# Kernel tuning notes

Measured on AMD Instinct MI355X. Metric: run time of the kernel, lower is better.

The kernel has to match this reference:

```python
import jax, jax.numpy as jnp
import numpy as np

N_HEAD = 12

def setup_inputs() -> dict:
    key = jax.random.key(0)
    k1, k2, k3 = jax.random.split(key, 3)
    B, T, C = 8, 1024, 768
    x = jax.random.normal(k1, (B, T, C), dtype=jnp.float32)
    # Linear weights stored as [in, out] so y = x @ W + b (same math as torch Linear)
    w_attn = jax.random.normal(k2, (C, 3 * C), dtype=jnp.float32) * (1.0 / np.sqrt(C))
    b_attn = jnp.zeros((3 * C,), dtype=jnp.float32)
    w_proj = jax.random.normal(k3, (C, C), dtype=jnp.float32) * (1.0 / np.sqrt(C))
    b_proj = jnp.zeros((C,), dtype=jnp.float32)
    return {"x": x, "w_attn": w_attn, "b_attn": b_attn, "w_proj": w_proj, "b_proj": b_proj}

def reference(x, w_attn, b_attn, w_proj, b_proj):
    B, T, C = x.shape
    H = N_HEAD
    D = C // H
    qkv = x @ w_attn + b_attn                        # [B,T,3C]
    q, k, v = jnp.split(qkv, 3, axis=-1)             # each [B,T,C]
    q = q.reshape(B, T, H, D).transpose(0, 2, 1, 3)  # [B,H,T,D]
    k = k.reshape(B, T, H, D).transpose(0, 2, 1, 3)
    v = v.reshape(B, T, H, D).transpose(0, 2, 1, 3)
    scale = 1.0 / jnp.sqrt(jnp.asarray(D, dtype=x.dtype))
    att = jnp.einsum('bhqd,bhkd->bhqk', q, k) * scale  # [B,H,T,T]
    causal = jnp.tril(jnp.ones((T, T), dtype=bool))    # [T,T]
    att = jnp.where(causal[None, None], att, jnp.asarray(-jnp.inf, dtype=att.dtype))
    att = jax.nn.softmax(att, axis=-1)
    out = jnp.einsum('bhqk,bhkd->bhqd', att, v)        # [B,H,T,D]
    out = out.transpose(0, 2, 1, 3).reshape(B, T, C)
    return out @ w_proj + b_proj
```

## Files before the change

### kernel.cpp

```cpp
#include <hip/hip_runtime.h>
#include <hip/hip_bf16.h>
#include <cmath>

#define B_ 8
#define T_ 1024
#define C_ 768
#define H_ 12
#define D_ 64
#define N3C 2304
#define M_ 8192

typedef __bf16 bf16x4 __attribute__((ext_vector_type(4)));
typedef __bf16 bf16x8 __attribute__((ext_vector_type(8)));
typedef float  f32x4  __attribute__((ext_vector_type(4)));

typedef const __attribute__((address_space(1))) void* gptr_t;
typedef __attribute__((address_space(3))) void* lptr_t;

#define LOG2E 1.44269504088896f

__device__ __forceinline__ bf16x8 cvt_bf16x8(const float4& a, const float4& b) {
    bf16x8 r;
    r[0] = (__bf16)a.x; r[1] = (__bf16)a.y; r[2] = (__bf16)a.z; r[3] = (__bf16)a.w;
    r[4] = (__bf16)b.x; r[5] = (__bf16)b.y; r[6] = (__bf16)b.z; r[7] = (__bf16)b.w;
    return r;
}

__global__ __launch_bounds__(256) void prepass(const float* __restrict__ x,
                                               __bf16* __restrict__ xb,
                                               const float* __restrict__ wa,
                                               __bf16* __restrict__ wat,
                                               const float* __restrict__ wp,
                                               __bf16* __restrict__ wpt) {
    __shared__ float tile[32][33];
    const int bx = blockIdx.x, tid = threadIdx.x;
    if (bx < 3072) {
        int i = (bx * 256 + tid) * 8;
        float4 a = *(const float4*)&x[i];
        float4 b = *(const float4*)&x[i + 4];
        *(bf16x8*)&xb[i] = cvt_bf16x8(a, b);
        return;
    }
    const float* w;
    __bf16* wt;
    int K, N, n0, k0;
    if (bx < 4800) {
        int bb = bx - 3072;
        w = wa; wt = wat; K = 768; N = 2304;
        n0 = (bb % 72) * 32; k0 = (bb / 72) * 32;
    } else {
        int bb = bx - 4800;
        w = wp; wt = wpt; K = 768; N = 768;
        n0 = (bb % 24) * 32; k0 = (bb / 24) * 32;
    }
    int tx = tid & 31, ty = tid >> 5;
#pragma unroll
    for (int i = 0; i < 4; i++)
        tile[ty + i * 8][tx] = w[(size_t)(k0 + ty + i * 8) * N + n0 + tx];
    __syncthreads();
#pragma unroll
    for (int i = 0; i < 4; i++)
        wt[(size_t)(n0 + ty + i * 8) * K + k0 + tx] = (__bf16)tile[tx][ty + i * 8];
}

__global__ __launch_bounds__(256) void qkv_gemm_mfma(const __bf16* __restrict__ A,
                                                     const __bf16* __restrict__ Bt,
                                                     const float* __restrict__ bias,
                                                     __bf16* __restrict__ qb,
                                                     __bf16* __restrict__ kb,
                                                     __bf16* __restrict__ vbt) {
    __shared__ __bf16 smem[128 * 136];
    __bf16* As = smem;
    __bf16* Bs = smem + 8192;
    const int tid = threadIdx.x;
    const int wave = tid >> 6, lane = tid & 63;
    const int lane15 = lane & 15, quad = lane >> 4;
    const int bid = blockIdx.x;
    const int m0 = ((bid & 7) * 8 + ((bid >> 3) & 7)) * 128;
    const int n0 = (bid >> 6) * 128;
    const int wm = (wave >> 1) * 64, wn = (wave & 1) * 64;
    f32x4 acc[4][4] = {};

#define QSTAGE(KC)                                                                  \
    {                                                                               \
        const int k0s = (KC) * 64;                                                  \
        _Pragma("unroll")                                                           \
        for (int r = 0; r < 4; ++r) {                                               \
            int p = r * 256 + tid;                                                  \
            int mrow = p >> 3, csw = p & 7;                                         \
            int ksrc = (csw ^ (mrow & 7)) * 8;                                      \
            __builtin_amdgcn_global_load_lds(                                       \
                (gptr_t)(A + (size_t)(m0 + mrow) * 768 + k0s + ksrc),               \
                (lptr_t)(As + (r * 256 + wave * 64) * 8), 16, 0, 0);                \
            __builtin_amdgcn_global_load_lds(                                       \
                (gptr_t)(Bt + (size_t)(n0 + mrow) * 768 + k0s + ksrc),              \
                (lptr_t)(Bs + (r * 256 + wave * 64) * 8), 16, 0, 0);                \
        }                                                                           \
    }

    for (int kc = 0; kc < 12; ++kc) {
        QSTAGE(kc);
        __syncthreads();
#pragma unroll
        for (int ks = 0; ks < 2; ++ks) {
            bf16x8 af[4], bf[4];
#pragma unroll
            for (int mt = 0; mt < 4; ++mt) {
                int m = wm + mt * 16 + lane15;
                int csw = (ks * 4 + quad) ^ (m & 7);
                af[mt] = *(const bf16x8*)(As + m * 64 + csw * 8);
            }
#pragma unroll
            for (int nt = 0; nt < 4; ++nt) {
                int n = wn + nt * 16 + lane15;
                int csw = (ks * 4 + quad) ^ (n & 7);
                bf[nt] = *(const bf16x8*)(Bs + n * 64 + csw * 8);
            }
#pragma unroll
            for (int mt = 0; mt < 4; ++mt)
#pragma unroll
                for (int nt = 0; nt < 4; ++nt)
                    acc[mt][nt] = __builtin_amdgcn_mfma_f32_16x16x32_bf16(af[mt], bf[nt], acc[mt][nt], 0, 0, 0);
        }
        __syncthreads();
    }

    if (n0 < 1536) {
        const bool isq = (n0 < 768);
        const float sc = isq ? (0.125f * LOG2E) : 1.0f;
#pragma unroll
        for (int nt = 0; nt < 4; ++nt) {
            int n = n0 + wn + nt * 16 + lane15;
            int rem = isq ? n : (n - 768);
            int h = rem >> 6;
            int d = n & 63;
            float bv = bias[n];
            __bf16* dst = isq ? qb : kb;
#pragma unroll
            for (int mt = 0; mt < 4; ++mt) {
#pragma unroll
                for (int reg = 0; reg < 4; ++reg) {
                    int mr = m0 + wm + mt * 16 + quad * 4 + reg;
                    int bb = mr >> 10, t = mr & 1023;
                    dst[(((size_t)bb * H_ + h) * T_ + t) * D_ + d] =
                        (__bf16)((acc[mt][nt][reg] + bv) * sc);
                }
            }
        }
    } else {
        __bf16* vls = smem;
#pragma unroll
        for (int nt = 0; nt < 4; ++nt) {
            int nl = wn + nt * 16 + lane15;
            float bv = bias[n0 + nl];
#pragma unroll
            for (int mt = 0; mt < 4; ++mt)
#pragma unroll
                for (int reg = 0; reg < 4; ++reg)
                    vls[nl * 136 + wm + mt * 16 + quad * 4 + reg] =
                        (__bf16)(acc[mt][nt][reg] + bv);
        }
        __syncthreads();
        int nl = tid >> 1;
        int t0 = (tid & 1) * 64;
        int n = n0 + nl;
        int h = (n - 1536) >> 6;
        int d = n & 63;
        int bb = m0 >> 10, tg = (m0 & 1023) + t0;
        __bf16* dst = vbt + (((size_t)bb * H_ + h) * D_ + d) * T_ + tg;
        const __bf16* srcl = vls + nl * 136 + t0;
#pragma unroll
        for (int c = 0; c < 8; ++c) {
            bf16x8 v;
#pragma unroll
            for (int i = 0; i < 8; ++i) {
                int s = c * 8 + i;
                v[i] = srcl[(s & 3) * 16 + (s >> 2)];
            }
            *(bf16x8*)(dst + c * 8) = v;
        }
    }
}

__global__ __launch_bounds__(256) void proj_gemm_mfma(const __bf16* __restrict__ A,
                                                      const __bf16* __restrict__ Bt,
                                                      const float* __restrict__ bias,
                                                      float* __restrict__ out) {
    __shared__ __bf16 As[128 * 64];
    __shared__ __bf16 Bs[64 * 64];
    const int tid = threadIdx.x;
    const int wave = tid >> 6, lane = tid & 63;
    const int lane15 = lane & 15, quad = lane >> 4;
    const int bid = blockIdx.x;
    const int m0 = ((bid & 7) * 8 + ((bid >> 3) & 7)) * 128;
    const int n0 = (bid >> 6) * 64;
    const int wm = wave * 32;
    f32x4 acc[2][4] = {};

#define PSTAGE(KC)                                                                  \
    {                                                                               \
        const int k0s = (KC) * 64;                                                  \
        _Pragma("unroll")                                                           \
        for (int r = 0; r < 4; ++r) {                                               \
            int p = r * 256 + tid;                                                  \
            int mrow = p >> 3, csw = p & 7;                                         \
            int ksrc = (csw ^ (mrow & 7)) * 8;                                      \
            __builtin_amdgcn_global_load_lds(                                       \
                (gptr_t)(A + (size_t)(m0 + mrow) * 768 + k0s + ksrc),               \
                (lptr_t)(&As[0] + (r * 256 + wave * 64) * 8), 16, 0, 0);            \
        }                                                                           \
        _Pragma("unroll")                                                           \
        for (int r = 0; r < 2; ++r) {                                               \
            int p = r * 256 + tid;                                                  \
            int nrow = p >> 3, csw = p & 7;                                         \
            int ksrc = (csw ^ (nrow & 7)) * 8;                                      \
            __builtin_amdgcn_global_load_lds(                                       \
                (gptr_t)(Bt + (size_t)(n0 + nrow) * 768 + k0s + ksrc),              \
                (lptr_t)(&Bs[0] + (r * 256 + wave * 64) * 8), 16, 0, 0);            \
        }                                                                           \
    }

    for (int kc = 0; kc < 12; ++kc) {
        PSTAGE(kc);
        __syncthreads();
#pragma unroll
        for (int ks = 0; ks < 2; ++ks) {
            bf16x8 af[2], bf[4];
#pragma unroll
            for (int mt = 0; mt < 2; ++mt) {
                int m = wm + mt * 16 + lane15;
                int csw = (ks * 4 + quad) ^ (m & 7);
                af[mt] = *(const bf16x8*)(&As[0] + m * 64 + csw * 8);
            }
#pragma unroll
            for (int nt = 0; nt < 4; ++nt) {
                int n = nt * 16 + lane15;
                int csw = (ks * 4 + quad) ^ (n & 7);
                bf[nt] = *(const bf16x8*)(&Bs[0] + n * 64 + csw * 8);
            }
#pragma unroll
            for (int mt = 0; mt < 2; ++mt)
#pragma unroll
                for (int nt = 0; nt < 4; ++nt)
                    acc[mt][nt] = __builtin_amdgcn_mfma_f32_16x16x32_bf16(af[mt], bf[nt], acc[mt][nt], 0, 0, 0);
        }
        __syncthreads();
    }

#pragma unroll
    for (int nt = 0; nt < 4; ++nt) {
        int n = n0 + nt * 16 + lane15;
        float bv = bias[n];
#pragma unroll
        for (int mt = 0; mt < 2; ++mt) {
#pragma unroll
            for (int reg = 0; reg < 4; ++reg) {
                int mr = m0 + wm + mt * 16 + quad * 4 + reg;
                out[(size_t)mr * C_ + n] = acc[mt][nt][reg] + bv;
            }
        }
    }
}

__global__ __launch_bounds__(256) void attn_mfma(const __bf16* __restrict__ qb,
                                                 const __bf16* __restrict__ kb,
                                                 const __bf16* __restrict__ vbt,
                                                 __bf16* __restrict__ ao) {
    __shared__ __bf16 Ks[2][64 * 64];
    __shared__ __bf16 Vts[2][64 * 64];
    __shared__ __bf16 Ps[4 * 32 * 72];

    const int tid = threadIdx.x;
    const int wave = tid >> 6, lane = tid & 63;
    const int lane15 = lane & 15, quad = lane >> 4;
    const int bh = blockIdx.x;
    const int qt = 7 - blockIdx.y;
    const int b = bh / H_, h = bh % H_;
    const int q0 = qt * 128;

    const __bf16* Kb = kb + (size_t)bh * T_ * D_;
    const __bf16* Vb = vbt + (size_t)bh * D_ * T_;
    __bf16* Pw = Ps + wave * 32 * 72;

    bf16x8 qf[2][2];
#pragma unroll
    for (int g = 0; g < 2; ++g) {
        const __bf16* qrow = qb + ((size_t)bh * T_ + q0 + wave * 32 + g * 16 + lane15) * D_ + quad * 8;
        qf[g][0] = *(const bf16x8*)qrow;
        qf[g][1] = *(const bf16x8*)(qrow + 32);
    }

    f32x4 o[2][4] = {};
    float lsum[2][4] = {};

    const int kunits = 2 * qt + 2;

#define ASTAGE(KU, BUF)                                                            \
    {                                                                              \
        const int k0s = (KU) * 64;                                                 \
        _Pragma("unroll")                                                          \
        for (int r = 0; r < 2; ++r) {                                              \
            int p = r * 256 + tid;                                                 \
            int row = p >> 3, c = p & 7;                                           \
            int cs = (c ^ (row & 7)) * 8;                                          \
            __builtin_amdgcn_global_load_lds(                                      \
                (gptr_t)(Kb + (size_t)(k0s + row) * D_ + cs),                      \
                (lptr_t)(&Ks[BUF][0] + (r * 256 + wave * 64) * 8), 16, 0, 0);      \
            __builtin_amdgcn_global_load_lds(                                      \
                (gptr_t)(Vb + (size_t)row * T_ + k0s + cs),                        \
                (lptr_t)(&Vts[BUF][0] + (r * 256 + wave * 64) * 8), 16, 0, 0);     \
        }                                                                          \
    }

    ASTAGE(0, 0);

    for (int ku = 0; ku < kunits; ++ku) {
        __syncthreads();
        if (ku + 1 < kunits) ASTAGE(ku + 1, (ku + 1) & 1);
        const __bf16* Kc = &Ks[ku & 1][0];
        const __bf16* Vc = &Vts[ku & 1][0];
        const int k0 = ku * 64;

        f32x4 s[2][4];
#pragma unroll
        for (int kt = 0; kt < 4; ++kt) {
            int row = kt * 16 + lane15;
            bf16x8 kf0 = *(const bf16x8*)(Kc + row * 64 + ((quad) ^ (row & 7)) * 8);
            bf16x8 kf1 = *(const bf16x8*)(Kc + row * 64 + ((4 + quad) ^ (row & 7)) * 8);
#pragma unroll
            for (int g = 0; g < 2; ++g) {
                f32x4 t = {};
                t = __builtin_amdgcn_mfma_f32_16x16x32_bf16(qf[g][0], kf0, t, 0, 0, 0);
                t = __builtin_amdgcn_mfma_f32_16x16x32_bf16(qf[g][1], kf1, t, 0, 0, 0);
                s[g][kt] = t;
            }
        }

        const bool diag = (ku >= 2 * qt);
#pragma unroll
        for (int g = 0; g < 2; ++g) {
#pragma unroll
            for (int r = 0; r < 4; ++r) {
                bf16x4 pk;
#pragma unroll
                for (int kt = 0; kt < 4; ++kt) {
                    int col = k0 + kt * 16 + lane15;
                    float p = __builtin_amdgcn_exp2f(s[g][kt][r]);
                    if (diag) {
                        int qrow = q0 + wave * 32 + g * 16 + quad * 4 + r;
                        if (col > qrow) p = 0.f;
                    }
                    lsum[g][r] += p;
                    pk[kt] = (__bf16)p;
                }
                *(bf16x4*)(Pw + (g * 16 + quad * 4 + r) * 72 + lane15 * 4) = pk;
            }
        }

        bf16x8 vf[4][2];
#pragma unroll
        for (int dt = 0; dt < 4; ++dt) {
            int row = dt * 16 + lane15;
#pragma unroll
            for (int half = 0; half < 2; ++half)
                vf[dt][half] = *(const bf16x8*)(Vc + row * 64 + ((half * 4 + quad) ^ (row & 7)) * 8);
        }
#pragma unroll
        for (int g = 0; g < 2; ++g) {
#pragma unroll
            for (int half = 0; half < 2; ++half) {
                bf16x8 pf = *(const bf16x8*)(Pw + (g * 16 + lane15) * 72 + half * 32 + quad * 8);
#pragma unroll
                for (int dt = 0; dt < 4; ++dt)
                    o[g][dt] = __builtin_amdgcn_mfma_f32_16x16x32_bf16(pf, vf[dt][half], o[g][dt], 0, 0, 0);
            }
        }
    }

#pragma unroll
    for (int g = 0; g < 2; ++g) {
        float inv[4];
#pragma unroll
        for (int r = 0; r < 4; ++r) {
            float ls = lsum[g][r];
            ls += __shfl_xor(ls, 1);
            ls += __shfl_xor(ls, 2);
            ls += __shfl_xor(ls, 4);
            ls += __shfl_xor(ls, 8);
            inv[r] = 1.0f / ls;
        }
#pragma unroll
        for (int dt = 0; dt < 4; ++dt) {
#pragma unroll
            for (int r = 0; r < 4; ++r) {
                int t = q0 + wave * 32 + g * 16 + quad * 4 + r;
                ao[((size_t)(b * T_ + t)) * C_ + h * 64 + dt * 16 + lane15] =
                    (__bf16)(o[g][dt][r] * inv[r]);
            }
        }
    }
}

extern "C" void kernel_launch(void* const* d_in, const int* in_sizes, int n_in,
                              void* d_out, int out_size, void* d_ws, size_t ws_size,
                              hipStream_t stream) {
    const float* x = (const float*)d_in[0];
    const float* w_attn = (const float*)d_in[1];
    const float* b_attn = (const float*)d_in[2];
    const float* w_proj = (const float*)d_in[3];
    const float* b_proj = (const float*)d_in[4];
    float* out = (float*)d_out;

    __bf16* xb = (__bf16*)d_ws;
    __bf16* wat = xb + (size_t)M_ * C_;
    __bf16* wpt = wat + (size_t)N3C * C_;
    __bf16* qb = wpt + (size_t)C_ * C_;
    __bf16* kb = qb + (size_t)96 * T_ * D_;
    __bf16* vbt = kb + (size_t)96 * T_ * D_;
    __bf16* ao = vbt + (size_t)96 * T_ * D_;

    prepass<<<5376, 256, 0, stream>>>(x, xb, w_attn, wat, w_proj, wpt);
    qkv_gemm_mfma<<<1152, 256, 0, stream>>>(xb, wat, b_attn, qb, kb, vbt);
    attn_mfma<<<dim3(96, 8), 256, 0, stream>>>(qb, kb, vbt, ao);
    proj_gemm_mfma<<<768, 256, 0, stream>>>(ao, wpt, b_proj, out);
}
```

Before: 182.7 us.

## Restructure QKV GEMM into 256x128 tiles with triple-buffered async LDS pipeline

The QKV projection GEMM now uses 512-thread blocks computing 256x128 tiles, with a three-stage LDS ring buffer filled by direct global-to-LDS loads two k-chunks ahead. The k-loop is split into four phases that interleave LDS fragment reads, prefetch issue, raw s_barrier and MFMA bursts under raised wave priority, with explicit vmcnt waits replacing full __syncthreads. The block index mapping is re-swizzled for the new grid. The goal is to hide global load latency behind MFMA work and increase operand reuse, at the cost of much larger shared memory (144KB) and occupancy limited to at most two blocks per CU.

```diff
diff --git a/kernel.cpp b/kernel.cpp
--- a/kernel.cpp
+++ b/kernel.cpp
@@ -63,66 +63,132 @@
         wt[(size_t)(n0 + ty + i * 8) * K + k0 + tx] = (__bf16)tile[tx][ty + i * 8];
 }
 
-__global__ __launch_bounds__(256) void qkv_gemm_mfma(const __bf16* __restrict__ A,
-                                                     const __bf16* __restrict__ Bt,
-                                                     const float* __restrict__ bias,
-                                                     __bf16* __restrict__ qb,
-                                                     __bf16* __restrict__ kb,
-                                                     __bf16* __restrict__ vbt) {
-    __shared__ __bf16 smem[128 * 136];
-    __bf16* As = smem;
-    __bf16* Bs = smem + 8192;
+__global__ __launch_bounds__(512, 2) void qkv_gemm_mfma(const __bf16* __restrict__ A,
+                                                        const __bf16* __restrict__ Bt,
+                                                        const float* __restrict__ bias,
+                                                        __bf16* __restrict__ qb,
+                                                        __bf16* __restrict__ kb,
+                                                        __bf16* __restrict__ vbt) {
+    __shared__ __bf16 smem[73728];
+    __bf16* Abuf = smem;
+    __bf16* Bbuf = smem + 49152;
     const int tid = threadIdx.x;
     const int wave = tid >> 6, lane = tid & 63;
     const int lane15 = lane & 15, quad = lane >> 4;
-    const int bid = blockIdx.x;
-    const int m0 = ((bid & 7) * 8 + ((bid >> 3) & 7)) * 128;
-    const int n0 = (bid >> 6) * 128;
+    const int swz = (blockIdx.x & 7) * 72 + (blockIdx.x >> 3);
+    const int n0 = (swz % 18) * 128;
+    const int m0 = (swz / 18) * 256;
     const int wm = (wave >> 1) * 64, wn = (wave & 1) * 64;
     f32x4 acc[4][4] = {};
 
-#define QSTAGE(KC)                                                                  \
+#define ISSUE_A2(KC, R0)                                                            \
     {                                                                               \
         const int k0s = (KC) * 64;                                                  \
+        __bf16* Ad = Abuf + ((KC) % 3) * 16384;                                     \
         _Pragma("unroll")                                                           \
-        for (int r = 0; r < 4; ++r) {                                               \
-            int p = r * 256 + tid;                                                  \
-            int mrow = p >> 3, csw = p & 7;                                         \
-            int ksrc = (csw ^ (mrow & 7)) * 8;                                      \
+        for (int r = (R0); r < (R0) + 2; ++r) {                                     \
+            int p = r * 512 + tid;                                                  \
+            int row = p >> 3, csw = p & 7;                                          \
             __builtin_amdgcn_global_load_lds(                                       \
-                (gptr_t)(A + (size_t)(m0 + mrow) * 768 + k0s + ksrc),               \
-                (lptr_t)(As + (r * 256 + wave * 64) * 8), 16, 0, 0);                \
-            __builtin_amdgcn_global_load_lds(                                       \
-                (gptr_t)(Bt + (size_t)(n0 + mrow) * 768 + k0s + ksrc),              \
-                (lptr_t)(Bs + (r * 256 + wave * 64) * 8), 16, 0, 0);                \
+                (gptr_t)(A + (size_t)(m0 + row) * 768 + k0s + (csw ^ (row & 7)) * 8), \
+                (lptr_t)(Ad + (r * 512 + wave * 64) * 8), 16, 0, 0);                \
         }                                                                           \
     }
 
+#define ISSUE_B1(KC, R0)                                                            \
+    {                                                                               \
+        const int k0s = (KC) * 64;                                                  \
+        __bf16* Bd = Bbuf + ((KC) % 3) * 8192;                                      \
+        int p = (R0) * 512 + tid;                                                   \
+        int row = p >> 3, csw = p & 7;                                              \
+        __builtin_amdgcn_global_load_lds(                                           \
+            (gptr_t)(Bt + (size_t)(n0 + row) * 768 + k0s + (csw ^ (row & 7)) * 8),  \
+            (lptr_t)(Bd + ((R0) * 512 + wave * 64) * 8), 16, 0, 0);                 \
+    }
+
+#define BAR() asm volatile("s_barrier" ::: "memory")
+
+    ISSUE_A2(0, 0); ISSUE_A2(0, 2); ISSUE_B1(0, 0); ISSUE_B1(0, 1);
+    ISSUE_A2(1, 0); ISSUE_A2(1, 2); ISSUE_B1(1, 0); ISSUE_B1(1, 1);
+
     for (int kc = 0; kc < 12; ++kc) {
-        QSTAGE(kc);
-        __syncthreads();
-#pragma unroll
-        for (int ks = 0; ks < 2; ++ks) {
-            bf16x8 af[4], bf[4];
-#pragma unroll
-            for (int mt = 0; mt < 4; ++mt) {
-                int m = wm + mt * 16 + lane15;
-                int csw = (ks * 4 + quad) ^ (m & 7);
-                af[mt] = *(const bf16x8*)(As + m * 64 + csw * 8);
-            }
-#pragma unroll
-            for (int nt = 0; nt < 4; ++nt) {
-                int n = wn + nt * 16 + lane15;
-                int csw = (ks * 4 + quad) ^ (n & 7);
-                bf[nt] = *(const bf16x8*)(Bs + n * 64 + csw * 8);
-            }
-#pragma unroll
-            for (int mt = 0; mt < 4; ++mt)
-#pragma unroll
-                for (int nt = 0; nt < 4; ++nt)
-                    acc[mt][nt] = __builtin_amdgcn_mfma_f32_16x16x32_bf16(af[mt], bf[nt], acc[mt][nt], 0, 0, 0);
-        }
-        __syncthreads();
+        if (kc < 11) { asm volatile("s_waitcnt vmcnt(6)" ::: "memory"); }
+        else         { asm volatile("s_waitcnt vmcnt(0)" ::: "memory"); }
+        BAR();
+        const __bf16* Ac = Abuf + (kc % 3) * 16384;
+        const __bf16* Bc = Bbuf + (kc % 3) * 8192;
+        const bool pf = (kc + 2 < 12);
+
+        bf16x8 af[4], bfr[2];
+#pragma unroll
+        for (int mt = 0; mt < 4; ++mt) {
+            int m = wm + mt * 16 + lane15;
+            af[mt] = *(const bf16x8*)(Ac + m * 64 + (quad ^ (m & 7)) * 8);
+        }
+#pragma unroll
+        for (int nt = 0; nt < 2; ++nt) {
+            int n = wn + nt * 16 + lane15;
+            bfr[nt] = *(const bf16x8*)(Bc + n * 64 + (quad ^ (n & 7)) * 8);
+        }
+        if (pf) ISSUE_A2(kc + 2, 0);
+        BAR();
+        __builtin_amdgcn_s_setprio(1);
+#pragma unroll
+        for (int mt = 0; mt < 4; ++mt)
+#pragma unroll
+            for (int nt = 0; nt < 2; ++nt)
+                acc[mt][nt] = __builtin_amdgcn_mfma_f32_16x16x32_bf16(af[mt], bfr[nt], acc[mt][nt], 0, 0, 0);
+        __builtin_amdgcn_s_setprio(0);
+
+#pragma unroll
+        for (int nt = 0; nt < 2; ++nt) {
+            int n = wn + (2 + nt) * 16 + lane15;
+            bfr[nt] = *(const bf16x8*)(Bc + n * 64 + (quad ^ (n & 7)) * 8);
+        }
+        if (pf) ISSUE_A2(kc + 2, 2);
+        BAR();
+        __builtin_amdgcn_s_setprio(1);
+#pragma unroll
+        for (int mt = 0; mt < 4; ++mt)
+#pragma unroll
+            for (int nt = 0; nt < 2; ++nt)
+                acc[mt][2 + nt] = __builtin_amdgcn_mfma_f32_16x16x32_bf16(af[mt], bfr[nt], acc[mt][2 + nt], 0, 0, 0);
+        __builtin_amdgcn_s_setprio(0);
+
+#pragma unroll
+        for (int mt = 0; mt < 4; ++mt) {
+            int m = wm + mt * 16 + lane15;
+            af[mt] = *(const bf16x8*)(Ac + m * 64 + ((4 + quad) ^ (m & 7)) * 8);
+        }
+#pragma unroll
+        for (int nt = 0; nt < 2; ++nt) {
+            int n = wn + nt * 16 + lane15;
+            bfr[nt] = *(const bf16x8*)(Bc + n * 64 + ((4 + quad) ^ (n & 7)) * 8);
+        }
+        if (pf) ISSUE_B1(kc + 2, 0);
+        BAR();
+        __builtin_amdgcn_s_setprio(1);
+#pragma unroll
+        for (int mt = 0; mt < 4; ++mt)
+#pragma unroll
+            for (int nt = 0; nt < 2; ++nt)
+                acc[mt][nt] = __builtin_amdgcn_mfma_f32_16x16x32_bf16(af[mt], bfr[nt], acc[mt][nt], 0, 0, 0);
+        __builtin_amdgcn_s_setprio(0);
+
+#pragma unroll
+        for (int nt = 0; nt < 2; ++nt) {
+            int n = wn + (2 + nt) * 16 + lane15;
+            bfr[nt] = *(const bf16x8*)(Bc + n * 64 + ((4 + quad) ^ (n & 7)) * 8);
+        }
+        if (pf) ISSUE_B1(kc + 2, 1);
+        BAR();
+        __builtin_amdgcn_s_setprio(1);
+#pragma unroll
+        for (int mt = 0; mt < 4; ++mt)
+#pragma unroll
+            for (int nt = 0; nt < 2; ++nt)
+                acc[mt][2 + nt] = __builtin_amdgcn_mfma_f32_16x16x32_bf16(af[mt], bfr[nt], acc[mt][2 + nt], 0, 0, 0);
+        __builtin_amdgcn_s_setprio(0);
     }
 
     if (n0 < 1536) {
@@ -157,18 +223,18 @@
             for (int mt = 0; mt < 4; ++mt)
 #pragma unroll
                 for (int reg = 0; reg < 4; ++reg)
-                    vls[nl * 136 + wm + mt * 16 + quad * 4 + reg] =
+                    vls[nl * 264 + wm + mt * 16 + quad * 4 + reg] =
                         (__bf16)(acc[mt][nt][reg] + bv);
         }
         __syncthreads();
-        int nl = tid >> 1;
-        int t0 = (tid & 1) * 64;
+        int nl = tid >> 2;
+        int t0 = (tid & 3) * 64;
         int n = n0 + nl;
         int h = (n - 1536) >> 6;
         int d = n & 63;
         int bb = m0 >> 10, tg = (m0 & 1023) + t0;
         __bf16* dst = vbt + (((size_t)bb * H_ + h) * D_ + d) * T_ + tg;
-        const __bf16* srcl = vls + nl * 136 + t0;
+        const __bf16* srcl = vls + nl * 264 + t0;
 #pragma unroll
         for (int c = 0; c < 8; ++c) {
             bf16x8 v;
@@ -180,6 +246,9 @@
             *(bf16x8*)(dst + c * 8) = v;
         }
     }
+#undef ISSUE_A2
+#undef ISSUE_B1
+#undef BAR
 }
 
 __global__ __launch_bounds__(256) void proj_gemm_mfma(const __bf16* __restrict__ A,
@@ -420,7 +489,7 @@
     __bf16* ao = vbt + (size_t)96 * T_ * D_;
 
     prepass<<<5376, 256, 0, stream>>>(x, xb, w_attn, wat, w_proj, wpt);
-    qkv_gemm_mfma<<<1152, 256, 0, stream>>>(xb, wat, b_attn, qb, kb, vbt);
+    qkv_gemm_mfma<<<576, 512, 0, stream>>>(xb, wat, b_attn, qb, kb, vbt);
     attn_mfma<<<dim3(96, 8), 256, 0, stream>>>(qb, kb, vbt, ao);
     proj_gemm_mfma<<<768, 256, 0, stream>>>(ao, wpt, b_proj, out);
 }
```

Result: faster. 170.4 us (-6.7%).

## Triple-buffer QKV GEMM with async LDS loads and 256x128 tiles

Applied to the files above, without the earlier changes.

The QKV GEMM now uses 512-thread blocks computing 256x128 tiles, with a three-stage LDS ring filled by global_load_lds, so chunks kc+1 and kc+2 stream in while chunk kc is being computed. It waits on vmcnt with manual counts instead of double __syncthreads, raises wave priority around the MFMA section, and re-swizzles the block-to-tile mapping. This is meant to hide global load latency and improve reuse of A and B tiles. In exchange it uses about 144KB of LDS per block, which limits occupancy, and relies on hand-written waitcnt values being correct.

```diff
diff --git a/kernel.cpp b/kernel.cpp
--- a/kernel.cpp
+++ b/kernel.cpp
@@ -63,66 +63,80 @@
         wt[(size_t)(n0 + ty + i * 8) * K + k0 + tx] = (__bf16)tile[tx][ty + i * 8];
 }
 
-__global__ __launch_bounds__(256) void qkv_gemm_mfma(const __bf16* __restrict__ A,
-                                                     const __bf16* __restrict__ Bt,
-                                                     const float* __restrict__ bias,
-                                                     __bf16* __restrict__ qb,
-                                                     __bf16* __restrict__ kb,
-                                                     __bf16* __restrict__ vbt) {
-    __shared__ __bf16 smem[128 * 136];
-    __bf16* As = smem;
-    __bf16* Bs = smem + 8192;
+__global__ __launch_bounds__(512, 2) void qkv_gemm_mfma(const __bf16* __restrict__ A,
+                                                        const __bf16* __restrict__ Bt,
+                                                        const float* __restrict__ bias,
+                                                        __bf16* __restrict__ qb,
+                                                        __bf16* __restrict__ kb,
+                                                        __bf16* __restrict__ vbt) {
+    __shared__ __bf16 smem[73728];
+    __bf16* Abuf = smem;
+    __bf16* Bbuf = smem + 49152;
     const int tid = threadIdx.x;
     const int wave = tid >> 6, lane = tid & 63;
     const int lane15 = lane & 15, quad = lane >> 4;
-    const int bid = blockIdx.x;
-    const int m0 = ((bid & 7) * 8 + ((bid >> 3) & 7)) * 128;
-    const int n0 = (bid >> 6) * 128;
+    const int swz = (blockIdx.x & 7) * 72 + (blockIdx.x >> 3);
+    const int n0 = (swz % 18) * 128;
+    const int m0 = (swz / 18) * 256;
     const int wm = (wave >> 1) * 64, wn = (wave & 1) * 64;
     f32x4 acc[4][4] = {};
 
-#define QSTAGE(KC)                                                                  \
+#define ISSUE6(KC)                                                                  \
     {                                                                               \
         const int k0s = (KC) * 64;                                                  \
+        __bf16* Ad = Abuf + ((KC) % 3) * 16384;                                     \
+        __bf16* Bd = Bbuf + ((KC) % 3) * 8192;                                      \
         _Pragma("unroll")                                                           \
         for (int r = 0; r < 4; ++r) {                                               \
-            int p = r * 256 + tid;                                                  \
-            int mrow = p >> 3, csw = p & 7;                                         \
-            int ksrc = (csw ^ (mrow & 7)) * 8;                                      \
+            int p = r * 512 + tid;                                                  \
+            int row = p >> 3, csw = p & 7;                                          \
             __builtin_amdgcn_global_load_lds(                                       \
-                (gptr_t)(A + (size_t)(m0 + mrow) * 768 + k0s + ksrc),               \
-                (lptr_t)(As + (r * 256 + wave * 64) * 8), 16, 0, 0);                \
+                (gptr_t)(A + (size_t)(m0 + row) * 768 + k0s + (csw ^ (row & 7)) * 8), \
+                (lptr_t)(Ad + (r * 512 + wave * 64) * 8), 16, 0, 0);                \
+        }                                                                           \
+        _Pragma("unroll")                                                           \
+        for (int r = 0; r < 2; ++r) {                                               \
+            int p = r * 512 + tid;                                                  \
+            int row = p >> 3, csw = p & 7;                                          \
             __builtin_amdgcn_global_load_lds(                                       \
-                (gptr_t)(Bt + (size_t)(n0 + mrow) * 768 + k0s + ksrc),              \
-                (lptr_t)(Bs + (r * 256 + wave * 64) * 8), 16, 0, 0);                \
+                (gptr_t)(Bt + (size_t)(n0 + row) * 768 + k0s + (csw ^ (row & 7)) * 8), \
+                (lptr_t)(Bd + (r * 512 + wave * 64) * 8), 16, 0, 0);                \
         }                                                                           \
     }
 
+    ISSUE6(0);
+    ISSUE6(1);
+
     for (int kc = 0; kc < 12; ++kc) {
-        QSTAGE(kc);
-        __syncthreads();
+        if (kc < 11) { asm volatile("s_waitcnt vmcnt(6)" ::: "memory"); }
+        else         { asm volatile("s_waitcnt vmcnt(0)" ::: "memory"); }
+        asm volatile("s_barrier" ::: "memory");
+        if (kc + 2 < 12) ISSUE6(kc + 2);
+        const __bf16* Ac = Abuf + (kc % 3) * 16384;
+        const __bf16* Bc = Bbuf + (kc % 3) * 8192;
+        __builtin_amdgcn_s_setprio(1);
 #pragma unroll
         for (int ks = 0; ks < 2; ++ks) {
-            bf16x8 af[4], bf[4];
+            bf16x8 af[4], bfr[4];
 #pragma unroll
             for (int mt = 0; mt < 4; ++mt) {
                 int m = wm + mt * 16 + lane15;
                 int csw = (ks * 4 + quad) ^ (m & 7);
-                af[mt] = *(const bf16x8*)(As + m * 64 + csw * 8);
+                af[mt] = *(const bf16x8*)(Ac + m * 64 + csw * 8);
             }
 #pragma unroll
             for (int nt = 0; nt < 4; ++nt) {
                 int n = wn + nt * 16 + lane15;
                 int csw = (ks * 4 + quad) ^ (n & 7);
-                bf[nt] = *(const bf16x8*)(Bs + n * 64 + csw * 8);
+                bfr[nt] = *(const bf16x8*)(Bc + n * 64 + csw * 8);
             }
 #pragma unroll
             for (int mt = 0; mt < 4; ++mt)
 #pragma unroll
                 for (int nt = 0; nt < 4; ++nt)
-                    acc[mt][nt] = __builtin_amdgcn_mfma_f32_16x16x32_bf16(af[mt], bf[nt], acc[mt][nt], 0, 0, 0);
-        }
-        __syncthreads();
+                    acc[mt][nt] = __builtin_amdgcn_mfma_f32_16x16x32_bf16(af[mt], bfr[nt], acc[mt][nt], 0, 0, 0);
+        }
+        __builtin_amdgcn_s_setprio(0);
     }
 
     if (n0 < 1536) {
@@ -148,6 +162,7 @@
             }
         }
     } else {
+        __syncthreads();
         __bf16* vls = smem;
 #pragma unroll
         for (int nt = 0; nt < 4; ++nt) {
@@ -157,18 +172,18 @@
             for (int mt = 0; mt < 4; ++mt)
 #pragma unroll
                 for (int reg = 0; reg < 4; ++reg)
-                    vls[nl * 136 + wm + mt * 16 + quad * 4 + reg] =
+                    vls[nl * 264 + wm + mt * 16 + quad * 4 + reg] =
                         (__bf16)(acc[mt][nt][reg] + bv);
         }
         __syncthreads();
-        int nl = tid >> 1;
-        int t0 = (tid & 1) * 64;
+        int nl = tid >> 2;
+        int t0 = (tid & 3) * 64;
         int n = n0 + nl;
         int h = (n - 1536) >> 6;
         int d = n & 63;
         int bb = m0 >> 10, tg = (m0 & 1023) + t0;
         __bf16* dst = vbt + (((size_t)bb * H_ + h) * D_ + d) * T_ + tg;
-        const __bf16* srcl = vls + nl * 136 + t0;
+        const __bf16* srcl = vls + nl * 264 + t0;
 #pragma unroll
         for (int c = 0; c < 8; ++c) {
             bf16x8 v;
@@ -180,6 +195,7 @@
             *(bf16x8*)(dst + c * 8) = v;
         }
     }
+#undef ISSUE6
 }
 
 __global__ __launch_bounds__(256) void proj_gemm_mfma(const __bf16* __restrict__ A,
@@ -420,7 +436,7 @@
     __bf16* ao = vbt + (size_t)96 * T_ * D_;
 
     prepass<<<5376, 256, 0, stream>>>(x, xb, w_attn, wat, w_proj, wpt);
-    qkv_gemm_mfma<<<1152, 256, 0, stream>>>(xb, wat, b_attn, qb, kb, vbt);
+    qkv_gemm_mfma<<<576, 512, 0, stream>>>(xb, wat, b_attn, qb, kb, vbt);
     attn_mfma<<<dim3(96, 8), 256, 0, stream>>>(qb, kb, vbt, ao);
     proj_gemm_mfma<<<768, 256, 0, stream>>>(ao, wpt, b_proj, out);
 }
```

Result: no change. 180.3 us (-1.3%).
